# Optimization experiments

Measured on AMD Instinct MI355X. Metric: run time of the kernel, lower is better.

Reference implementation:

```python
import jax, jax.numpy as jnp
import numpy as np

N_NODES = 10000
IN_CH = 128
OUT_CH = 128
N_EDGES = 320000


def setup_inputs() -> dict:
    key = jax.random.key(0)
    k1, k2, k3, k4 = jax.random.split(key, 4)
    x = jax.random.normal(k1, (N_NODES, IN_CH), dtype=jnp.float32)
    edge_index = jax.random.randint(k2, (N_EDGES, 2), 0, N_NODES, dtype=jnp.int64)
    # Linear weights (torch stores [out, in]); scale like kaiming-uniform-ish
    w = jax.random.normal(k3, (OUT_CH, IN_CH), dtype=jnp.float32) / np.sqrt(IN_CH)
    b = jax.random.normal(k4, (OUT_CH, IN_CH), dtype=jnp.float32) / np.sqrt(IN_CH)
    return {"x": x, "edge_index": edge_index, "w": w, "b": b}


def reference(x, edge_index, w, b):
    n = x.shape[0]
    # Each edge (i, j) contributes x[j] to node i and x[i] to node j (undirected).
    src = jnp.concatenate([edge_index[:, 1], edge_index[:, 0]])  # feature source
    dst = jnp.concatenate([edge_index[:, 0], edge_index[:, 1]])  # aggregation target
    # segment-sum of gathered neighbor features -> [n, in_ch]
    agg_sum = jax.ops.segment_sum(x[src], dst, num_segments=n)
    deg = jax.ops.segment_sum(jnp.ones_like(dst, dtype=x.dtype), dst, num_segments=n)
    # mean with zero fallback for isolated nodes (original uses zeros vector)
    agg = jnp.where(deg[:, None] > 0, agg_sum / jnp.maximum(deg, 1.0)[:, None], 0.0)
    # out = ReLU(agg @ w^T + x @ b^T)
    return jax.nn.relu(agg @ w.T + x @ b.T)
```

## Files before the change

### kernel.cpp

```cpp
#include <hip/hip_runtime.h>

#define N_NODES 10000
#define CH 128
#define N_EDGES 320000
#define CAP 128
#define CSTR 16

#define FILL_BLOCKS ((N_EDGES + 255) / 256)
#define CONV_THREADS (N_NODES * CH / 8)
#define CONV_BLOCKS ((CONV_THREADS + 255) / 256)
#define PACK_THREADS (128 * 128)
#define PACK_BLOCKS (PACK_THREADS / 256)
#define KSEG 5
#define WBK (KSEG * CH)


typedef __attribute__((ext_vector_type(8))) short short8v;
typedef __attribute__((ext_vector_type(4))) float floatx4;

__device__ __forceinline__ unsigned short f2bf(float f) {
    unsigned u = __float_as_uint(f);
    return (unsigned short)((u + 0x7FFFu + ((u >> 16) & 1u)) >> 16);
}
__device__ __forceinline__ float bf2f(unsigned short h) {
    return __uint_as_float(((unsigned)h) << 16);
}

__global__ __launch_bounds__(256) void fill_conv_pack_kernel(const int* __restrict__ ei,
                                                             int* __restrict__ cursor,
                                                             unsigned short* __restrict__ adj,
                                                             const float* __restrict__ x,
                                                             unsigned short* __restrict__ xhi,
                                                             unsigned short* __restrict__ xlo,
                                                             const float* __restrict__ w,
                                                             const float* __restrict__ b,
                                                             unsigned short* __restrict__ wbt)
{
    const int bid = blockIdx.x;
    if (bid < FILL_BLOCKS) {
        const int t = bid * 256 + threadIdx.x;
        if (t >= N_EDGES) return;
        const int2 p = ((const int2*)ei)[t];
        if ((unsigned)p.x >= N_NODES || (unsigned)p.y >= N_NODES) return;
        const int s0 = atomicAdd(&cursor[p.x * CSTR], 1);
        const int s1 = atomicAdd(&cursor[p.y * CSTR], 1);
        if (s0 < CAP) adj[(size_t)p.x * CAP + s0] = (unsigned short)p.y;
        if (s1 < CAP) adj[(size_t)p.y * CAP + s1] = (unsigned short)p.x;
    } else if (bid < FILL_BLOCKS + CONV_BLOCKS) {
        const int t = (bid - FILL_BLOCKS) * 256 + threadIdx.x;
        const float4 a = ((const float4*)x)[t * 2];
        const float4 c = ((const float4*)x)[t * 2 + 1];
        ushort4 h0, h1, l0, l1;
        h0.x = f2bf(a.x); l0.x = f2bf(a.x - bf2f(h0.x));
        h0.y = f2bf(a.y); l0.y = f2bf(a.y - bf2f(h0.y));
        h0.z = f2bf(a.z); l0.z = f2bf(a.z - bf2f(h0.z));
        h0.w = f2bf(a.w); l0.w = f2bf(a.w - bf2f(h0.w));
        h1.x = f2bf(c.x); l1.x = f2bf(c.x - bf2f(h1.x));
        h1.y = f2bf(c.y); l1.y = f2bf(c.y - bf2f(h1.y));
        h1.z = f2bf(c.z); l1.z = f2bf(c.z - bf2f(h1.z));
        h1.w = f2bf(c.w); l1.w = f2bf(c.w - bf2f(h1.w));
        ((ushort4*)xhi)[t * 2]     = h0;
        ((ushort4*)xhi)[t * 2 + 1] = h1;
        ((ushort4*)xlo)[t * 2]     = l0;
        ((ushort4*)xlo)[t * 2 + 1] = l1;
    } else {
        const int t = (bid - FILL_BLOCKS - CONV_BLOCKS) * 256 + threadIdx.x;
        const int n = t >> 7;
        const int k = t & 127;
        const float wv = w[n * CH + k];
        const float bv = b[n * CH + k];
        const unsigned short whi = f2bf(wv);
        const unsigned short wlo = f2bf(wv - bf2f(whi));
        const unsigned short bhi = f2bf(bv);
        const unsigned short blo = f2bf(bv - bf2f(bhi));
        unsigned short* row = wbt + (size_t)n * WBK;
        row[k]          = whi;
        row[CH + k]     = wlo;
        row[2 * CH + k] = bhi;
        row[3 * CH + k] = blo;
        row[4 * CH + k] = bhi;
    }
}

__global__ __launch_bounds__(256) void gather_kernel(const unsigned short* __restrict__ xhi,
                                                     const int* __restrict__ cursor,
                                                     const unsigned short* __restrict__ adj,
                                                     unsigned short* __restrict__ aggb)
{
    const int wv   = threadIdx.x >> 6;
    const int node = blockIdx.x * 4 + wv;
    const int lane = threadIdx.x & 63;
    const int h    = lane >> 5;
    const int l    = lane & 31;

    const int deg = cursor[node * CSTR];
    const int d   = deg < CAP ? deg : CAP;
    const unsigned short* nb = adj + (size_t)node * CAP;

    float4 acc = {0.f, 0.f, 0.f, 0.f};
    const int nit = (d + 1) >> 1;
#pragma unroll 4
    for (int it = 0; it < nit; ++it) {
        const int idx = 2 * it + h;
        int j = nb[idx];
        j = j < N_NODES ? j : 0;
        const ushort4 u = ((const ushort4*)(xhi + (size_t)j * CH))[l];
        const float m = idx < d ? 1.0f : 0.0f;
        acc.x += m * bf2f(u.x);
        acc.y += m * bf2f(u.y);
        acc.z += m * bf2f(u.z);
        acc.w += m * bf2f(u.w);
    }
    acc.x += __shfl_xor(acc.x, 32, 64);
    acc.y += __shfl_xor(acc.y, 32, 64);
    acc.z += __shfl_xor(acc.z, 32, 64);
    acc.w += __shfl_xor(acc.w, 32, 64);

    if (h == 0) {
        const float inv = deg > 0 ? 1.0f / (float)deg : 0.0f;
        ushort4 o;
        o.x = f2bf(acc.x * inv);
        o.y = f2bf(acc.y * inv);
        o.z = f2bf(acc.z * inv);
        o.w = f2bf(acc.w * inv);
        ((ushort4*)(aggb + (size_t)node * CH))[l] = o;
    }
}

__global__ __launch_bounds__(256) void mfma_gemm_kernel(const unsigned short* __restrict__ aggb,
                                                        const unsigned short* __restrict__ xhi,
                                                        const unsigned short* __restrict__ xlo,
                                                        const unsigned short* __restrict__ wbt,
                                                        float* __restrict__ out)
{
    const int wv    = threadIdx.x >> 6;
    const int lane  = threadIdx.x & 63;
    const int W     = blockIdx.x * 4 + wv;
    const int mtile = W >> 2;
    const int n0    = (W & 3) * 32;
    const int r     = lane & 15;
    const int q     = lane >> 4;
    const int arow  = mtile * 16 + r;

    floatx4 acc0 = {0.f, 0.f, 0.f, 0.f};
    floatx4 acc1 = {0.f, 0.f, 0.f, 0.f};

#pragma unroll
    for (int seg = 0; seg < KSEG; ++seg) {
        const unsigned short* A = (seg < 2) ? aggb : ((seg < 4) ? xhi : xlo);
        const int wk = seg * CH;
#pragma unroll
        for (int ks = 0; ks < 4; ++ks) {
            const int k0 = ks * 32 + q * 8;
            const short8v af  = *(const short8v*)(A + (size_t)arow * CH + k0);
            const short8v bf0 = *(const short8v*)(wbt + (size_t)(n0 + r) * WBK + wk + k0);
            const short8v bf1 = *(const short8v*)(wbt + (size_t)(n0 + 16 + r) * WBK + wk + k0);
            acc0 = __builtin_amdgcn_mfma_f32_16x16x32_bf16(af, bf0, acc0, 0, 0, 0);
            acc1 = __builtin_amdgcn_mfma_f32_16x16x32_bf16(af, bf1, acc1, 0, 0, 0);
        }
    }

    const int mbase = mtile * 16 + q * 4;
#pragma unroll
    for (int rr = 0; rr < 4; ++rr) {
        float v0 = acc0[rr];
        float v1 = acc1[rr];
        v0 = v0 > 0.f ? v0 : 0.f;
        v1 = v1 > 0.f ? v1 : 0.f;
        out[(size_t)(mbase + rr) * CH + n0 + r]      = v0;
        out[(size_t)(mbase + rr) * CH + n0 + 16 + r] = v1;
    }
}

extern "C" void kernel_launch(void* const* d_in, const int* in_sizes, int n_in,
                              void* d_out, int out_size, void* d_ws, size_t ws_size,
                              hipStream_t stream)
{
    const float* x  = (const float*)d_in[0];
    const int*   ei = (const int*)d_in[1];
    const float* w  = (const float*)d_in[2];
    const float* b  = (const float*)d_in[3];
    float*       out = (float*)d_out;

    int*            cursor = (int*)d_ws;
    unsigned short* adj    = (unsigned short*)((char*)d_ws + 640000);
    unsigned short* xhi    = (unsigned short*)((char*)d_ws + 3200000);
    unsigned short* xlo    = (unsigned short*)((char*)d_ws + 5760000);
    unsigned short* aggb   = (unsigned short*)((char*)d_ws + 8320000);
    unsigned short* wbt    = (unsigned short*)((char*)d_ws + 10880000);

    hipMemsetAsync(d_ws, 0, (size_t)N_NODES * CSTR * sizeof(int), stream);

    fill_conv_pack_kernel<<<FILL_BLOCKS + CONV_BLOCKS + PACK_BLOCKS, 256, 0, stream>>>(
        ei, cursor, adj, x, xhi, xlo, w, b, wbt);
    gather_kernel<<<N_NODES / 4, 256, 0, stream>>>(xhi, cursor, adj, aggb);
    mfma_gemm_kernel<<<625, 256, 0, stream>>>(aggb, xhi, xlo, wbt, out);
}
```

Measured before the change: 131.6 us.

## Batch edge fill per thread, widen gather loads, split GEMM waves per 16 columns

The fill stage now has each thread process four edges through two int4 loads instead of one edge via int2. The gather kernel moves to 16-byte loads per lane, with four neighbours in flight per wave and a two-stage shuffle reduction. The GEMM kernel gives each wave a single 16-column tile and doubles the grid, trading per-wave A-fragment reuse for more waves and fewer registers. These changes aim to cut memory instruction count and raise parallelism, at the cost of more redundant A loads in the GEMM.

```diff
diff --git a/kernel.cpp b/kernel.cpp
--- a/kernel.cpp
+++ b/kernel.cpp
@@ -6,7 +6,8 @@
 #define CAP 128
 #define CSTR 16
 
-#define FILL_BLOCKS ((N_EDGES + 255) / 256)
+#define EPT 4
+#define FILL_BLOCKS ((N_EDGES / EPT + 255) / 256)
 #define CONV_THREADS (N_NODES * CH / 8)
 #define CONV_BLOCKS ((CONV_THREADS + 255) / 256)
 #define PACK_THREADS (128 * 128)
@@ -39,13 +40,20 @@
     const int bid = blockIdx.x;
     if (bid < FILL_BLOCKS) {
         const int t = bid * 256 + threadIdx.x;
-        if (t >= N_EDGES) return;
-        const int2 p = ((const int2*)ei)[t];
-        if ((unsigned)p.x >= N_NODES || (unsigned)p.y >= N_NODES) return;
-        const int s0 = atomicAdd(&cursor[p.x * CSTR], 1);
-        const int s1 = atomicAdd(&cursor[p.y * CSTR], 1);
-        if (s0 < CAP) adj[(size_t)p.x * CAP + s0] = (unsigned short)p.y;
-        if (s1 < CAP) adj[(size_t)p.y * CAP + s1] = (unsigned short)p.x;
+        if (t >= N_EDGES / EPT) return;
+        const int4 e01 = ((const int4*)ei)[t * 2];
+        const int4 e23 = ((const int4*)ei)[t * 2 + 1];
+        const int px[4] = {e01.x, e01.z, e23.x, e23.z};
+        const int py[4] = {e01.y, e01.w, e23.y, e23.w};
+#pragma unroll
+        for (int e = 0; e < 4; ++e) {
+            const int a = px[e], c = py[e];
+            if ((unsigned)a >= N_NODES || (unsigned)c >= N_NODES) continue;
+            const int s0 = atomicAdd(&cursor[a * CSTR], 1);
+            const int s1 = atomicAdd(&cursor[c * CSTR], 1);
+            if (s0 < CAP) adj[(size_t)a * CAP + s0] = (unsigned short)c;
+            if (s1 < CAP) adj[(size_t)c * CAP + s1] = (unsigned short)a;
+        }
     } else if (bid < FILL_BLOCKS + CONV_BLOCKS) {
         const int t = (bid - FILL_BLOCKS) * 256 + threadIdx.x;
         const float4 a = ((const float4*)x)[t * 2];
@@ -90,40 +98,57 @@
     const int wv   = threadIdx.x >> 6;
     const int node = blockIdx.x * 4 + wv;
     const int lane = threadIdx.x & 63;
-    const int h    = lane >> 5;
-    const int l    = lane & 31;
+    const int h    = lane >> 4;
+    const int l    = lane & 15;
 
     const int deg = cursor[node * CSTR];
     const int d   = deg < CAP ? deg : CAP;
     const unsigned short* nb = adj + (size_t)node * CAP;
 
-    float4 acc = {0.f, 0.f, 0.f, 0.f};
-    const int nit = (d + 1) >> 1;
+    float4 accA = {0.f, 0.f, 0.f, 0.f};
+    float4 accB = {0.f, 0.f, 0.f, 0.f};
+    const int nit = (d + 3) >> 2;
 #pragma unroll 4
     for (int it = 0; it < nit; ++it) {
-        const int idx = 2 * it + h;
+        const int idx = 4 * it + h;
         int j = nb[idx];
         j = j < N_NODES ? j : 0;
-        const ushort4 u = ((const ushort4*)(xhi + (size_t)j * CH))[l];
+        const uint4 q = ((const uint4*)(xhi + (size_t)j * CH))[l];
         const float m = idx < d ? 1.0f : 0.0f;
-        acc.x += m * bf2f(u.x);
-        acc.y += m * bf2f(u.y);
-        acc.z += m * bf2f(u.z);
-        acc.w += m * bf2f(u.w);
-    }
-    acc.x += __shfl_xor(acc.x, 32, 64);
-    acc.y += __shfl_xor(acc.y, 32, 64);
-    acc.z += __shfl_xor(acc.z, 32, 64);
-    acc.w += __shfl_xor(acc.w, 32, 64);
+        accA.x += m * __uint_as_float(q.x << 16);
+        accA.y += m * __uint_as_float(q.x & 0xffff0000u);
+        accA.z += m * __uint_as_float(q.y << 16);
+        accA.w += m * __uint_as_float(q.y & 0xffff0000u);
+        accB.x += m * __uint_as_float(q.z << 16);
+        accB.y += m * __uint_as_float(q.z & 0xffff0000u);
+        accB.z += m * __uint_as_float(q.w << 16);
+        accB.w += m * __uint_as_float(q.w & 0xffff0000u);
+    }
+    accA.x += __shfl_xor(accA.x, 16, 64);
+    accA.y += __shfl_xor(accA.y, 16, 64);
+    accA.z += __shfl_xor(accA.z, 16, 64);
+    accA.w += __shfl_xor(accA.w, 16, 64);
+    accB.x += __shfl_xor(accB.x, 16, 64);
+    accB.y += __shfl_xor(accB.y, 16, 64);
+    accB.z += __shfl_xor(accB.z, 16, 64);
+    accB.w += __shfl_xor(accB.w, 16, 64);
+    accA.x += __shfl_xor(accA.x, 32, 64);
+    accA.y += __shfl_xor(accA.y, 32, 64);
+    accA.z += __shfl_xor(accA.z, 32, 64);
+    accA.w += __shfl_xor(accA.w, 32, 64);
+    accB.x += __shfl_xor(accB.x, 32, 64);
+    accB.y += __shfl_xor(accB.y, 32, 64);
+    accB.z += __shfl_xor(accB.z, 32, 64);
+    accB.w += __shfl_xor(accB.w, 32, 64);
 
     if (h == 0) {
         const float inv = deg > 0 ? 1.0f / (float)deg : 0.0f;
-        ushort4 o;
-        o.x = f2bf(acc.x * inv);
-        o.y = f2bf(acc.y * inv);
-        o.z = f2bf(acc.z * inv);
-        o.w = f2bf(acc.w * inv);
-        ((ushort4*)(aggb + (size_t)node * CH))[l] = o;
+        uint4 o;
+        o.x = (unsigned)f2bf(accA.x * inv) | ((unsigned)f2bf(accA.y * inv) << 16);
+        o.y = (unsigned)f2bf(accA.z * inv) | ((unsigned)f2bf(accA.w * inv) << 16);
+        o.z = (unsigned)f2bf(accB.x * inv) | ((unsigned)f2bf(accB.y * inv) << 16);
+        o.w = (unsigned)f2bf(accB.z * inv) | ((unsigned)f2bf(accB.w * inv) << 16);
+        ((uint4*)(aggb + (size_t)node * CH))[l] = o;
     }
 }
 
@@ -136,14 +161,14 @@
     const int wv    = threadIdx.x >> 6;
     const int lane  = threadIdx.x & 63;
     const int W     = blockIdx.x * 4 + wv;
-    const int mtile = W >> 2;
-    const int n0    = (W & 3) * 32;
+    const int mtile = W >> 3;
+    const int n0    = (W & 7) * 16;
     const int r     = lane & 15;
     const int q     = lane >> 4;
     const int arow  = mtile * 16 + r;
 
-    floatx4 acc0 = {0.f, 0.f, 0.f, 0.f};
-    floatx4 acc1 = {0.f, 0.f, 0.f, 0.f};
+    const unsigned short* brow = wbt + (size_t)(n0 + r) * WBK;
+    floatx4 acc = {0.f, 0.f, 0.f, 0.f};
 
 #pragma unroll
     for (int seg = 0; seg < KSEG; ++seg) {
@@ -152,23 +177,18 @@
 #pragma unroll
         for (int ks = 0; ks < 4; ++ks) {
             const int k0 = ks * 32 + q * 8;
-            const short8v af  = *(const short8v*)(A + (size_t)arow * CH + k0);
-            const short8v bf0 = *(const short8v*)(wbt + (size_t)(n0 + r) * WBK + wk + k0);
-            const short8v bf1 = *(const short8v*)(wbt + (size_t)(n0 + 16 + r) * WBK + wk + k0);
-            acc0 = __builtin_amdgcn_mfma_f32_16x16x32_bf16(af, bf0, acc0, 0, 0, 0);
-            acc1 = __builtin_amdgcn_mfma_f32_16x16x32_bf16(af, bf1, acc1, 0, 0, 0);
+            const short8v af = *(const short8v*)(A + (size_t)arow * CH + k0);
+            const short8v bf = *(const short8v*)(brow + wk + k0);
+            acc = __builtin_amdgcn_mfma_f32_16x16x32_bf16(af, bf, acc, 0, 0, 0);
         }
     }
 
     const int mbase = mtile * 16 + q * 4;
 #pragma unroll
     for (int rr = 0; rr < 4; ++rr) {
-        float v0 = acc0[rr];
-        float v1 = acc1[rr];
-        v0 = v0 > 0.f ? v0 : 0.f;
-        v1 = v1 > 0.f ? v1 : 0.f;
-        out[(size_t)(mbase + rr) * CH + n0 + r]      = v0;
-        out[(size_t)(mbase + rr) * CH + n0 + 16 + r] = v1;
+        float v = acc[rr];
+        v = v > 0.f ? v : 0.f;
+        out[(size_t)(mbase + rr) * CH + n0 + r] = v;
     }
 }
 
@@ -194,5 +214,5 @@
     fill_conv_pack_kernel<<<FILL_BLOCKS + CONV_BLOCKS + PACK_BLOCKS, 256, 0, stream>>>(
         ei, cursor, adj, x, xhi, xlo, w, b, wbt);
     gather_kernel<<<N_NODES / 4, 256, 0, stream>>>(xhi, cursor, adj, aggb);
-    mfma_gemm_kernel<<<625, 256, 0, stream>>>(aggb, xhi, xlo, wbt, out);
-}
+    mfma_gemm_kernel<<<1250, 256, 0, stream>>>(aggb, xhi, xlo, wbt, out);
+}
```

Result: no change. 132.5 us (+0.7%).
